# Performance work log

Measured on AMD Instinct MI355X. Metric: run time of the kernel, lower is better.

The kernel has to match this reference:

```python
import math
import jax, jax.numpy as jnp
import numpy as np

V_NODES = 100000
E_EDGES = 800000
D_IN = 128
D_OUT = 128
H = 4
F_H = D_OUT // H
LEAK = 0.2


def _xavier(key, shape):
    fan_in, fan_out = shape[0], shape[1]
    lim = math.sqrt(6.0 / (fan_in + fan_out))
    return jax.random.uniform(key, shape, jnp.float32, -lim, lim)


def setup_inputs() -> dict:
    key = jax.random.key(0)
    ks = jax.random.split(key, 10)
    h = jax.random.normal(ks[0], (V_NODES, D_IN), jnp.float32)
    edge_index = jax.random.randint(ks[1], (2, E_EDGES), 0, V_NODES, jnp.int64)
    # omega in {+1, -1, 0}
    edge_weight = jax.random.randint(ks[2], (E_EDGES,), -1, 2).astype(jnp.float32)
    return {
        "h": h,
        "edge_index": edge_index,
        "edge_weight": edge_weight,
        "Wq": _xavier(ks[3], (D_IN, D_OUT)), "bq": jnp.zeros((D_OUT,), jnp.float32),
        "Wk": _xavier(ks[4], (D_IN, D_OUT)), "bk": jnp.zeros((D_OUT,), jnp.float32),
        "Wv": _xavier(ks[5], (D_IN, D_OUT)), "bv": jnp.zeros((D_OUT,), jnp.float32),
        "Wo": _xavier(ks[6], (D_OUT, D_OUT)), "bo": jnp.zeros((D_OUT,), jnp.float32),
        "We": _xavier(ks[7], (1, H)), "be": jnp.zeros((H,), jnp.float32),
        "gamma": jnp.ones((D_OUT,), jnp.float32), "beta": jnp.zeros((D_OUT,), jnp.float32),
    }


def _layer_norm(x, gamma, beta, eps=1e-5):
    mu = jnp.mean(x, axis=-1, keepdims=True)
    var = jnp.var(x, axis=-1, keepdims=True)
    return (x - mu) * jax.lax.rsqrt(var + eps) * gamma + beta


def reference(h, edge_index, edge_weight, Wq, bq, Wk, bk, Wv, bv, Wo, bo, We, be, gamma, beta):
    V = h.shape[0]
    Q = (h @ Wq + bq).reshape(V, H, F_H)
    K = (h @ Wk + bk).reshape(V, H, F_H)
    Vv = (h @ Wv + bv).reshape(V, H, F_H)

    src, tgt = edge_index[0], edge_index[1]
    # edge-aware bias: Proj(omega) with LeakyReLU, [E, H]
    edge_bias = jax.nn.leaky_relu(edge_weight[:, None] * We[0] + be, LEAK)

    # per-edge multi-head scores [E, H]
    attn_raw = jnp.einsum("ehf,ehf->eh", Q[src], K[tgt]) / math.sqrt(F_H)
    attn_raw = attn_raw + edge_bias  # ent_bias = 0 (add_entity_sim=False)
    attn_exp = jnp.exp(attn_raw)

    # degree-based softmax normalization over incoming edges of each target
    deg = jax.ops.segment_sum(attn_exp, tgt, num_segments=V) + 1e-16  # [V, H]
    attn_norm = attn_exp / deg[tgt]  # [E, H]  (dropout rate = 0)

    # weighted message aggregation: alpha * omega * (W_v h_src)
    msg = Vv[src] * attn_norm[:, :, None] * edge_weight[:, None, None]  # [E, H, F_H]
    out = jax.ops.segment_sum(msg, tgt, num_segments=V).reshape(V, H * F_H)

    out = out @ Wo + bo + h  # residual
    out = _layer_norm(out, gamma, beta)
    return jax.nn.leaky_relu(out, LEAK)
```

## Files before the change

kernel.cpp:

```cpp
#include <hip/hip_runtime.h>
#include <math.h>

#define V_NODES 100000
#define E_EDGES 800000
#define HEADS 4
#define FH 32
#define D 128
#define LEAK 0.2f
#define NB 8

__global__ __launch_bounds__(384) void qkv_kernel(
    const float* __restrict__ h,
    const float* __restrict__ Wq, const float* __restrict__ bq,
    const float* __restrict__ Wk, const float* __restrict__ bk,
    const float* __restrict__ Wv, const float* __restrict__ bv,
    float* __restrict__ Q, float* __restrict__ K, float* __restrict__ Vv)
{
    __shared__ float hsh[D][NB];
    const int tid  = threadIdx.x;
    const int base = blockIdx.x * NB;

    for (int idx = tid; idx < NB * D; idx += 384) {
        int n = idx >> 7, k = idx & 127;
        hsh[k][n] = h[(long)(base + n) * D + k];
    }
    __syncthreads();

    const int wsel = tid >> 7;
    const int col  = tid & 127;
    const float* W = (wsel == 0) ? Wq : (wsel == 1) ? Wk : Wv;
    const float* b = (wsel == 0) ? bq : (wsel == 1) ? bk : bv;
    float* O       = (wsel == 0) ? Q  : (wsel == 1) ? K  : Vv;

    float acc[NB];
#pragma unroll
    for (int n = 0; n < NB; n++) acc[n] = 0.f;

    for (int k = 0; k < D; k++) {
        float w = W[k * D + col];
#pragma unroll
        for (int n = 0; n < NB; n++) acc[n] += hsh[k][n] * w;
    }

    float bias = b[col];
#pragma unroll
    for (int n = 0; n < NB; n++) O[(long)(base + n) * D + col] = acc[n] + bias;
}

__global__ __launch_bounds__(256) void score_kernel(
    const int* __restrict__ src, const int* __restrict__ tgt,
    const float* __restrict__ ew,
    const float* __restrict__ Q, const float* __restrict__ K,
    const float* __restrict__ We, const float* __restrict__ be,
    float* __restrict__ attn_exp, float* __restrict__ deg)
{
    int e = blockIdx.x * 256 + threadIdx.x;
    if (e >= E_EDGES) return;
    int s = src[e], t = tgt[e];
    float w = ew[e];
    const float4* q4 = (const float4*)(Q + (long)s * D);
    const float4* k4 = (const float4*)(K + (long)t * D);

    float outv[HEADS];
#pragma unroll
    for (int hh = 0; hh < HEADS; hh++) {
        float dot = 0.f;
#pragma unroll
        for (int i = 0; i < 8; i++) {
            float4 a = q4[hh * 8 + i];
            float4 b = k4[hh * 8 + i];
            dot += a.x * b.x + a.y * b.y + a.z * b.z + a.w * b.w;
        }
        float bias = w * We[hh] + be[hh];
        bias = (bias > 0.f) ? bias : LEAK * bias;
        float sc = dot * 0.17677669529663687f + bias;
        outv[hh] = __expf(sc);
    }
    *((float4*)(attn_exp + (long)e * 4)) = make_float4(outv[0], outv[1], outv[2], outv[3]);
#pragma unroll
    for (int hh = 0; hh < HEADS; hh++) atomicAdd(&deg[t * 4 + hh], outv[hh]);
}

__global__ __launch_bounds__(256) void agg_kernel(
    const int* __restrict__ src, const int* __restrict__ tgt,
    const float* __restrict__ ew,
    const float* __restrict__ Vv, const float* __restrict__ attn_exp,
    const float* __restrict__ deg, float* __restrict__ out)
{
    long gid = (long)blockIdx.x * 256 + threadIdx.x;
    int e = (int)(gid >> 7);
    int c = (int)(gid & 127);
    float w = ew[e];
    if (w == 0.f) return;
    int t = tgt[e];
    int hh = c >> 5;
    float a = attn_exp[(long)e * 4 + hh] / (deg[t * 4 + hh] + 1e-16f) * w;
    float m = a * Vv[(long)src[e] * D + c];
    atomicAdd(&out[(long)t * D + c], m);
}

__global__ __launch_bounds__(128) void out_kernel(
    const float* __restrict__ h, const float* __restrict__ Wo,
    const float* __restrict__ bo, const float* __restrict__ gamma,
    const float* __restrict__ beta, float* __restrict__ out)
{
    __shared__ float ash[D][NB];
    __shared__ float red[2][NB][2];
    const int tid  = threadIdx.x;
    const int base = blockIdx.x * NB;
    const int wave = tid >> 6, lane = tid & 63;

#pragma unroll
    for (int n = 0; n < NB; n++) ash[tid][n] = out[(long)(base + n) * D + tid];
    __syncthreads();

    float acc[NB];
#pragma unroll
    for (int n = 0; n < NB; n++) acc[n] = 0.f;
    for (int k = 0; k < D; k++) {
        float w = Wo[k * D + tid];
#pragma unroll
        for (int n = 0; n < NB; n++) acc[n] += ash[k][n] * w;
    }

    float bb = bo[tid];
    float v[NB];
#pragma unroll
    for (int n = 0; n < NB; n++) {
        v[n] = acc[n] + bb + h[(long)(base + n) * D + tid];
        float s = v[n], q = v[n] * v[n];
#pragma unroll
        for (int off = 32; off; off >>= 1) {
            s += __shfl_xor(s, off);
            q += __shfl_xor(q, off);
        }
        if (lane == 0) { red[wave][n][0] = s; red[wave][n][1] = q; }
    }
    __syncthreads();

    float g = gamma[tid], bt = beta[tid];
#pragma unroll
    for (int n = 0; n < NB; n++) {
        float s  = red[0][n][0] + red[1][n][0];
        float q  = red[0][n][1] + red[1][n][1];
        float mu = s * (1.f / 128.f);
        float var = q * (1.f / 128.f) - mu * mu;
        float rstd = rsqrtf(var + 1e-5f);
        float y = (v[n] - mu) * rstd * g + bt;
        out[(long)(base + n) * D + tid] = (y > 0.f) ? y : LEAK * y;
    }
}

extern "C" void kernel_launch(void* const* d_in, const int* in_sizes, int n_in,
                              void* d_out, int out_size, void* d_ws, size_t ws_size,
                              hipStream_t stream)
{
    const float* h     = (const float*)d_in[0];
    const int*   ei    = (const int*)d_in[1];
    const float* ew    = (const float*)d_in[2];
    const float* Wq    = (const float*)d_in[3];
    const float* bq    = (const float*)d_in[4];
    const float* Wk    = (const float*)d_in[5];
    const float* bk    = (const float*)d_in[6];
    const float* Wv    = (const float*)d_in[7];
    const float* bv    = (const float*)d_in[8];
    const float* Wo    = (const float*)d_in[9];
    const float* bo    = (const float*)d_in[10];
    const float* We    = (const float*)d_in[11];
    const float* be    = (const float*)d_in[12];
    const float* gamma = (const float*)d_in[13];
    const float* beta  = (const float*)d_in[14];
    float* out = (float*)d_out;

    float* Q        = (float*)d_ws;
    float* K        = Q  + (size_t)V_NODES * D;
    float* Vv       = K  + (size_t)V_NODES * D;
    float* attn_exp = Vv + (size_t)V_NODES * D;
    float* deg      = attn_exp + (size_t)E_EDGES * 4;

    const int* srcp = ei;
    const int* tgtp = ei + E_EDGES;

    hipMemsetAsync(out, 0, (size_t)V_NODES * D * sizeof(float), stream);
    hipMemsetAsync(deg, 0, (size_t)V_NODES * HEADS * sizeof(float), stream);

    qkv_kernel<<<V_NODES / NB, 384, 0, stream>>>(h, Wq, bq, Wk, bk, Wv, bv, Q, K, Vv);
    score_kernel<<<E_EDGES / 256, 256, 0, stream>>>(srcp, tgtp, ew, Q, K, We, be, attn_exp, deg);
    agg_kernel<<<(int)((long)E_EDGES * D / 256), 256, 0, stream>>>(srcp, tgtp, ew, Vv, attn_exp, deg, out);
    out_kernel<<<V_NODES / NB, 128, 0, stream>>>(h, Wo, bo, gamma, beta, out);
}
```

Measured before the change: 898.4 us.

## Build CSR by target and aggregate per node without atomics

```diff
diff --git a/kernel.cpp b/kernel.cpp
--- a/kernel.cpp
+++ b/kernel.cpp
@@ -52,51 +52,100 @@
     const float* __restrict__ ew,
     const float* __restrict__ Q, const float* __restrict__ K,
     const float* __restrict__ We, const float* __restrict__ be,
-    float* __restrict__ attn_exp, float* __restrict__ deg)
+    float* __restrict__ attn_exp)
+{
+    int t = blockIdx.x * 256 + threadIdx.x;
+    int e = t >> 4;
+    int sub = t & 15;
+    if (e >= E_EDGES) return;
+    int s = src[e], tg = tgt[e];
+    const float4* q4 = (const float4*)(Q + (long)s * D);
+    const float4* k4 = (const float4*)(K + (long)tg * D);
+    float4 a0 = q4[sub * 2], a1 = q4[sub * 2 + 1];
+    float4 b0 = k4[sub * 2], b1 = k4[sub * 2 + 1];
+    float p = a0.x * b0.x + a0.y * b0.y + a0.z * b0.z + a0.w * b0.w
+            + a1.x * b1.x + a1.y * b1.y + a1.z * b1.z + a1.w * b1.w;
+    p += __shfl_xor(p, 1);
+    p += __shfl_xor(p, 2);
+    if ((sub & 3) == 0) {
+        int hh = sub >> 2;
+        float w = ew[e];
+        float bias = w * We[hh] + be[hh];
+        bias = (bias > 0.f) ? bias : LEAK * bias;
+        attn_exp[(long)e * 4 + hh] = __expf(p * 0.17677669529663687f + bias);
+    }
+}
+
+__global__ __launch_bounds__(256) void hist_kernel(
+    const int* __restrict__ tgt, int* __restrict__ rs)
+{
+    int e = blockIdx.x * 256 + threadIdx.x;
+    if (e < E_EDGES) atomicAdd(&rs[tgt[e]], 1);
+}
+
+__global__ __launch_bounds__(1024) void scan_kernel(int* __restrict__ rs)
+{
+    __shared__ int part[1024];
+    const int tid = threadIdx.x;
+    const int CH = (V_NODES + 1023) / 1024;
+    int begin = tid * CH;
+    int end   = begin + CH; if (end > V_NODES) end = V_NODES;
+    if (begin > V_NODES) begin = V_NODES;
+    int s = 0;
+    for (int i = begin; i < end; i++) s += rs[i];
+    part[tid] = s;
+    __syncthreads();
+    for (int off = 1; off < 1024; off <<= 1) {
+        int v = (tid >= off) ? part[tid - off] : 0;
+        __syncthreads();
+        part[tid] += v;
+        __syncthreads();
+    }
+    int excl = (tid == 0) ? 0 : part[tid - 1];
+    for (int i = begin; i < end; i++) {
+        int c = rs[i];
+        rs[i] = excl;
+        excl += c;
+    }
+}
+
+__global__ __launch_bounds__(256) void scatter_kernel(
+    const int* __restrict__ tgt, int* __restrict__ rs, int* __restrict__ csr_e)
 {
     int e = blockIdx.x * 256 + threadIdx.x;
     if (e >= E_EDGES) return;
-    int s = src[e], t = tgt[e];
-    float w = ew[e];
-    const float4* q4 = (const float4*)(Q + (long)s * D);
-    const float4* k4 = (const float4*)(K + (long)t * D);
-
-    float outv[HEADS];
-#pragma unroll
-    for (int hh = 0; hh < HEADS; hh++) {
-        float dot = 0.f;
-#pragma unroll
-        for (int i = 0; i < 8; i++) {
-            float4 a = q4[hh * 8 + i];
-            float4 b = k4[hh * 8 + i];
-            dot += a.x * b.x + a.y * b.y + a.z * b.z + a.w * b.w;
+    int pos = atomicAdd(&rs[tgt[e]], 1);
+    csr_e[pos] = e;
+}
+
+__global__ __launch_bounds__(256) void agg_kernel(
+    const int* __restrict__ rs, const int* __restrict__ csr_e,
+    const int* __restrict__ src, const float* __restrict__ ew,
+    const float* __restrict__ attn_exp,
+    const float* __restrict__ Vv, float* __restrict__ out)
+{
+    int node = blockIdx.x * 4 + (threadIdx.x >> 6);
+    if (node >= V_NODES) return;
+    int lane = threadIdx.x & 63;
+    int hh = lane >> 4;
+    int j1 = rs[node];
+    int j0 = node ? rs[node - 1] : 0;
+    float acc0 = 0.f, acc1 = 0.f, deg = 0.f;
+    for (int j = j0; j < j1; j++) {
+        int e = csr_e[j];
+        float4 att = *((const float4*)(attn_exp + (long)e * 4));
+        float atth = (hh == 0) ? att.x : (hh == 1) ? att.y : (hh == 2) ? att.z : att.w;
+        deg += atth;
+        float w = ew[e];
+        if (w != 0.f) {
+            float2 v = ((const float2*)(Vv + (long)src[e] * D))[lane];
+            float a = atth * w;
+            acc0 += a * v.x;
+            acc1 += a * v.y;
         }
-        float bias = w * We[hh] + be[hh];
-        bias = (bias > 0.f) ? bias : LEAK * bias;
-        float sc = dot * 0.17677669529663687f + bias;
-        outv[hh] = __expf(sc);
-    }
-    *((float4*)(attn_exp + (long)e * 4)) = make_float4(outv[0], outv[1], outv[2], outv[3]);
-#pragma unroll
-    for (int hh = 0; hh < HEADS; hh++) atomicAdd(&deg[t * 4 + hh], outv[hh]);
-}
-
-__global__ __launch_bounds__(256) void agg_kernel(
-    const int* __restrict__ src, const int* __restrict__ tgt,
-    const float* __restrict__ ew,
-    const float* __restrict__ Vv, const float* __restrict__ attn_exp,
-    const float* __restrict__ deg, float* __restrict__ out)
-{
-    long gid = (long)blockIdx.x * 256 + threadIdx.x;
-    int e = (int)(gid >> 7);
-    int c = (int)(gid & 127);
-    float w = ew[e];
-    if (w == 0.f) return;
-    int t = tgt[e];
-    int hh = c >> 5;
-    float a = attn_exp[(long)e * 4 + hh] / (deg[t * 4 + hh] + 1e-16f) * w;
-    float m = a * Vv[(long)src[e] * D + c];
-    atomicAdd(&out[(long)t * D + c], m);
+    }
+    float inv = 1.f / (deg + 1e-16f);
+    ((float2*)(out + (long)node * D))[lane] = make_float2(acc0 * inv, acc1 * inv);
 }
 
 __global__ __launch_bounds__(128) void out_kernel(
@@ -176,16 +225,21 @@
     float* K        = Q  + (size_t)V_NODES * D;
     float* Vv       = K  + (size_t)V_NODES * D;
     float* attn_exp = Vv + (size_t)V_NODES * D;
-    float* deg      = attn_exp + (size_t)E_EDGES * 4;
+
+    int* rs    = (int*)Q;
+    int* csr_e = rs + V_NODES;
 
     const int* srcp = ei;
     const int* tgtp = ei + E_EDGES;
 
-    hipMemsetAsync(out, 0, (size_t)V_NODES * D * sizeof(float), stream);
-    hipMemsetAsync(deg, 0, (size_t)V_NODES * HEADS * sizeof(float), stream);
-
     qkv_kernel<<<V_NODES / NB, 384, 0, stream>>>(h, Wq, bq, Wk, bk, Wv, bv, Q, K, Vv);
-    score_kernel<<<E_EDGES / 256, 256, 0, stream>>>(srcp, tgtp, ew, Q, K, We, be, attn_exp, deg);
-    agg_kernel<<<(int)((long)E_EDGES * D / 256), 256, 0, stream>>>(srcp, tgtp, ew, Vv, attn_exp, deg, out);
+    score_kernel<<<(E_EDGES * 16) / 256, 256, 0, stream>>>(srcp, tgtp, ew, Q, K, We, be, attn_exp);
+
+    hipMemsetAsync(rs, 0, V_NODES * sizeof(int), stream);
+    hist_kernel<<<(E_EDGES + 255) / 256, 256, 0, stream>>>(tgtp, rs);
+    scan_kernel<<<1, 1024, 0, stream>>>(rs);
+    scatter_kernel<<<(E_EDGES + 255) / 256, 256, 0, stream>>>(tgtp, rs, csr_e);
+
+    agg_kernel<<<(V_NODES + 3) / 4, 256, 0, stream>>>(rs, csr_e, srcp, ew, attn_exp, Vv, out);
     out_kernel<<<V_NODES / NB, 128, 0, stream>>>(h, Wo, bo, gamma, beta, out);
 }
```

Measured after the change: 911.9 us. Within noise of the previous version (+1.5%).
